# Kernel optimization log

Measured on AMD Instinct MI355X. Metric: run time of the kernel, lower is better.

## Reference

```python
import jax, jax.numpy as jnp
import numpy as np

WIN = 7                      # window_size[0] == window_size[1]
N_TOK = WIN * WIN            # 49 tokens per window
PRETRAIN = 12                # pretrain_window_size
LOG8 = float(np.log(8.0))


def _relative_position_index():
    # tf.meshgrid default 'xy' indexing == np.meshgrid default
    gh, gw = np.meshgrid(np.arange(WIN), np.arange(WIN))
    coords = np.stack([gh, gw], 0).reshape(2, -1)            # [2, N]
    rel = coords[:, :, None] - coords[:, None, :]            # [2, N, N]
    rel = rel.transpose(1, 2, 0)                             # [N, N, 2]
    ry = (rel[..., 0] + WIN - 1) * (2 * WIN - 1)
    rx = rel[..., 1] + WIN - 1
    return jnp.asarray((ry + rx).reshape(-1), dtype=jnp.int32)   # [N*N]


def _relative_coords_table():
    ch = np.arange(-(WIN - 1), WIN, dtype=np.float32)
    gh, gw = np.meshgrid(ch, ch)                             # 'xy' indexing
    t = np.stack([gh, gw], axis=-1)[None]                    # [1, 2W-1, 2W-1, 2]
    t = t / (PRETRAIN - 1)                                   # first divide
    t = t * (8.0 / (PRETRAIN - 1))                           # scale (as in source)
    t = np.sign(t) * np.log1p(np.abs(t)) / LOG8
    return jnp.asarray(t, dtype=jnp.float32)


REL_IDX = _relative_position_index()
COORDS_TABLE = _relative_coords_table()


def _l2_normalize(t, eps=1e-12):
    return t * jax.lax.rsqrt(jnp.maximum(jnp.sum(t * t, axis=-1, keepdims=True), eps))


def setup_inputs() -> dict:
    key = jax.random.key(0)
    ks = jax.random.split(key, 12)
    Bw, N, C, H, RPE_H = 2048, N_TOK, 512, 16, 512
    s = 0.02
    return {
        "x": jax.random.normal(ks[0], (Bw, N, C), jnp.float32),
        "mask": jax.random.normal(ks[1], (64, N, N), jnp.float32),
        "qkv_w": jax.random.normal(ks[2], (C, 3 * C), jnp.float32) * s,
        "q_bias": jnp.zeros((C,), jnp.float32),
        "v_bias": jnp.zeros((C,), jnp.float32),
        "logit_scale": jnp.full((H, 1, 1), np.log(10.0), jnp.float32),
        "rpe_w1": jax.random.normal(ks[3], (2, RPE_H), jnp.float32) * s,
        "rpe_b1": jnp.zeros((RPE_H,), jnp.float32),
        "rpe_w2": jax.random.normal(ks[4], (RPE_H, H), jnp.float32) * s,
        "proj_w": jax.random.normal(ks[5], (C, C), jnp.float32) * s,
        "proj_b": jnp.zeros((C,), jnp.float32),
    }


def reference(x, mask, qkv_w, q_bias, v_bias, logit_scale,
              rpe_w1, rpe_b1, rpe_w2, proj_w, proj_b):
    Bw, N, C = x.shape
    H = logit_scale.shape[0]
    hd = C // H

    qkv_bias = jnp.concatenate([q_bias, jnp.zeros_like(v_bias), v_bias])
    qkv = x @ qkv_w + qkv_bias                          # [Bw, N, 3C]
    qkv = qkv.reshape(Bw, N, 3, H, hd).transpose(2, 0, 3, 1, 4)
    q, k, v = qkv[0], qkv[1], qkv[2]                    # [Bw, H, N, hd]

    scale = jnp.exp(jnp.minimum(logit_scale, jnp.log(1.0 / 0.01)))  # [H,1,1]
    q = _l2_normalize(q)
    k = _l2_normalize(k)
    attn = jnp.einsum('bhnd,bhmd->bhnm', q, k) * scale  # [Bw, H, N, N]

    # RPE MLP on the (2W-1)^2 coords table, then gather per token pair
    h1 = jax.nn.relu(COORDS_TABLE @ rpe_w1 + rpe_b1)
    bias_table = (h1 @ rpe_w2).reshape(-1, H)           # [(2W-1)^2, H]
    pb = bias_table[REL_IDX].reshape(N, N, H).transpose(2, 0, 1)  # [H, N, N]
    attn = attn + 16.0 * jax.nn.sigmoid(pb)[None]

    nW = mask.shape[0]
    attn = attn.reshape(Bw // nW, nW, H, N, N) + mask[None, :, None]
    attn = attn.reshape(Bw, H, N, N)

    attn = jax.nn.softmax(attn, axis=-1)
    out = jnp.einsum('bhnm,bhmd->bnhd', attn, v).reshape(Bw, N, C)
    return out @ proj_w + proj_b
```

## Files before the change

### kernel.cpp

```cpp
#include <hip/hip_runtime.h>
#include <cstdint>

#define NTOK 49
#define CDIM 512
#define BW 2048
#define MROWS (BW * NTOK)
#define QKVN 1536

typedef __attribute__((ext_vector_type(4))) float f32x4;
typedef __attribute__((ext_vector_type(8))) short s16x8;
typedef __attribute__((ext_vector_type(2))) unsigned int u32x2;

__device__ __forceinline__ uint16_t f2b(float f) {
  uint32_t u = __float_as_uint(f);
  u += 0x7fffu + ((u >> 16) & 1u);
  return (uint16_t)(u >> 16);
}
__device__ __forceinline__ float b2f(uint16_t h) {
  return __uint_as_float(((uint32_t)h) << 16);
}

#define GLOAD_LDS16(gp, lp)                                                    \
  __builtin_amdgcn_global_load_lds(                                            \
      (__attribute__((address_space(1))) void*)(gp),                           \
      (__attribute__((address_space(3))) void*)(lp), 16, 0, 0)

__global__ __launch_bounds__(256) void cvt_x_kernel(const float* __restrict__ x,
                                                    uint16_t* __restrict__ xb) {
  long i = ((long)blockIdx.x * 256 + threadIdx.x) * 4;
  f32x4 v = *(const f32x4*)(x + i);
  uint64_t p = (uint64_t)f2b(v[0]) | ((uint64_t)f2b(v[1]) << 16) |
               ((uint64_t)f2b(v[2]) << 32) | ((uint64_t)f2b(v[3]) << 48);
  *(uint64_t*)(xb + i) = p;
}

__global__ __launch_bounds__(256) void prep_weights(
    const float* __restrict__ qkv_w, const float* __restrict__ proj_w,
    const float* __restrict__ q_bias, const float* __restrict__ v_bias,
    uint16_t* __restrict__ qkv_wT, uint16_t* __restrict__ proj_wT,
    float* __restrict__ qkv_bias) {
  int i = blockIdx.x * 256 + threadIdx.x;
  if (i < QKVN * CDIM) {
    int nn = i / CDIM, kk = i % CDIM;
    qkv_wT[i] = f2b(qkv_w[(long)kk * QKVN + nn]);
  }
  if (i < CDIM * CDIM) {
    int nn = i / CDIM, kk = i % CDIM;
    proj_wT[i] = f2b(proj_w[(long)kk * CDIM + nn]);
  }
  if (i < QKVN) {
    float bv = (i < 512) ? q_bias[i] : (i < 1024 ? 0.f : v_bias[i - 1024]);
    qkv_bias[i] = bv;
  }
}

__global__ __launch_bounds__(256) void rpe_table(const float* __restrict__ w1,
                                                 const float* __restrict__ b1,
                                                 const float* __restrict__ w2,
                                                 float* __restrict__ bias16) {
  int i = blockIdx.x * 256 + threadIdx.x;
  if (i >= 169 * 16) return;
  int f = i >> 4, h = i & 15;
  float d0 = (float)((f % 13) - 6);
  float d1 = (float)((f / 13) - 6);
  const float inv_log8 = 0.4808983469629878f;
  float v0 = (d0 / 11.0f) * (8.0f / 11.0f);
  float v1 = (d1 / 11.0f) * (8.0f / 11.0f);
  float f0 = copysignf(log1pf(fabsf(v0)) * inv_log8, v0);
  if (v0 == 0.f) f0 = 0.f;
  float f1 = copysignf(log1pf(fabsf(v1)) * inv_log8, v1);
  if (v1 == 0.f) f1 = 0.f;
  float acc = 0.f;
  for (int k = 0; k < 512; ++k) {
    float h1 = fmaxf(f0 * w1[k] + f1 * w1[512 + k] + b1[k], 0.f);
    acc += h1 * w2[k * 16 + h];
  }
  bias16[i] = 16.f / (1.f + expf(-acc));
}

__global__ __launch_bounds__(256) void build_tiles(
    const float* __restrict__ mask, const float* __restrict__ bias16,
    float* __restrict__ mask_t, float* __restrict__ bias_t) {
  int bid = blockIdx.x;
  int l = threadIdx.x >> 2, j = threadIdx.x & 3;
  int gg = l >> 4, cc = l & 15;
  if (bid < 1024) {
    int w = bid >> 4, tile = bid & 15;
    int mt = tile >> 2, nt = tile & 3;
    int q = nt * 16 + cc, k = mt * 16 + gg * 4 + j;
    float v;
    if (k >= 49) v = -1e30f;
    else if (q >= 49) v = 0.f;
    else v = mask[(long)w * 2401 + q * 49 + k];
    mask_t[(long)bid * 256 + threadIdx.x] = v;
  } else {
    int idx = bid - 1024;
    int h = idx >> 4, tile = idx & 15;
    int mt = tile >> 2, nt = tile & 3;
    int q = nt * 16 + cc, k = mt * 16 + gg * 4 + j;
    float v = 0.f;
    if (q < 49 && k < 49) {
      int ridx = (q % 7 - k % 7 + 6) * 13 + (q / 7 - k / 7 + 6);
      v = bias16[ridx * 16 + h];
    }
    bias_t[(long)idx * 256 + threadIdx.x] = v;
  }
}


#define STAGE_A(tile, half, buf)                                               \
  {                                                                            \
    const uint16_t* s_ = srcA + (half) * (128L * 512) + (long)(tile) * 64;     \
    uint16_t* d_ = &lds[(buf) * 32768 + (half) * 8192 + tid * 8];              \
    GLOAD_LDS16(s_, d_);                                                       \
    GLOAD_LDS16(s_ + 64 * 512, d_ + 4096);                                     \
  }

#define STAGE_B(tile, half, buf)                                               \
  {                                                                            \
    const uint16_t* s_ = srcB + (half) * (128L * 512) + (long)(tile) * 64;     \
    uint16_t* d_ = &lds[(buf) * 32768 + 16384 + (half) * 8192 + tid * 8];      \
    GLOAD_LDS16(s_, d_);                                                       \
    GLOAD_LDS16(s_ + 64 * 512, d_ + 4096);                                     \
  }

#define VM4 asm volatile("s_waitcnt vmcnt(4)" ::: "memory");
#define VM0 asm volatile("s_waitcnt vmcnt(0)" ::: "memory");

#define PHASE(buf, q, STAGES, TAIL)                                            \
  {                                                                            \
    s16x8 a00 = *(const s16x8*)&lds[(buf)*32768 + arow + (2*(q))*1024 + ax0];  \
    s16x8 a01 = *(const s16x8*)&lds[(buf)*32768 + arow + (2*(q))*1024 + ax1];  \
    s16x8 a10 = *(const s16x8*)&lds[(buf)*32768 + arow + (2*(q)+1)*1024 + ax0];\
    s16x8 a11 = *(const s16x8*)&lds[(buf)*32768 + arow + (2*(q)+1)*1024 + ax1];\
    if ((q) == 0) {                                                            \
      _Pragma("unroll")                                                        \
      for (int nf = 0; nf < 4; ++nf) {                                         \
        bfr0[nf] = *(const s16x8*)&lds[(buf)*32768 + brow_ + nf*1024 + ax0];   \
        bfr1[nf] = *(const s16x8*)&lds[(buf)*32768 + brow_ + nf*1024 + ax1];   \
      }                                                                        \
    }                                                                          \
    STAGES                                                                     \
    __builtin_amdgcn_s_barrier();                                              \
    asm volatile("s_waitcnt lgkmcnt(0)" ::: "memory");                         \
    __builtin_amdgcn_sched_barrier(0);                                         \
    __builtin_amdgcn_s_setprio(1);                                             \
    _Pragma("unroll")                                                          \
    for (int nf = 0; nf < 4; ++nf) {                                           \
      acc[2*(q)][nf] = __builtin_amdgcn_mfma_f32_16x16x32_bf16(                \
          a00, bfr0[nf], acc[2*(q)][nf], 0, 0, 0);                             \
      acc[2*(q)][nf] = __builtin_amdgcn_mfma_f32_16x16x32_bf16(                \
          a01, bfr1[nf], acc[2*(q)][nf], 0, 0, 0);                             \
      acc[2*(q)+1][nf] = __builtin_amdgcn_mfma_f32_16x16x32_bf16(              \
          a10, bfr0[nf], acc[2*(q)+1][nf], 0, 0, 0);                           \
      acc[2*(q)+1][nf] = __builtin_amdgcn_mfma_f32_16x16x32_bf16(              \
          a11, bfr1[nf], acc[2*(q)+1][nf], 0, 0, 0);                           \
    }                                                                          \
    __builtin_amdgcn_s_setprio(0);                                             \
    TAIL                                                                       \
    __builtin_amdgcn_s_barrier();                                              \
  }

template <int EPI>
__global__ __launch_bounds__(512, 2) void gemm8p(const uint16_t* __restrict__ A,
                                                 const uint16_t* __restrict__ BT,
                                                 const float* __restrict__ bias,
                                                 void* __restrict__ Cout,
                                                 int N, int ntn) {
  __shared__ uint16_t lds[2 * 32768];
  const int tid = threadIdx.x;
  const int wave = tid >> 6, lane = tid & 63;
  const int wm = wave >> 2, wn = wave & 3;
  const int c = lane & 15, g = lane >> 4;

  const int bid = blockIdx.x;
  const int nwg = gridDim.x;
  const int wg = (bid & 7) * (nwg >> 3) + (bid >> 3);
  const int mt = wg / ntn, nt = wg % ntn;
  const long brow = (long)mt * 256;
  const int bcol = nt * 256;

  const int lr0 = tid >> 3;
  const int chunk = tid & 7;
  const int scol = (chunk ^ (lr0 & 7)) * 8;
  const uint16_t* srcA = A + (brow + lr0) * 512 + scol;
  const uint16_t* srcB = BT + ((long)bcol + lr0) * 512 + scol;

  const int arow = wm * 8192 + c * 64;
  const int brow_ = 16384 + (wn >> 1) * 8192 + ((wn & 1) * 64 + c) * 64;
  const int ax0 = (g * 8) ^ ((c & 7) * 8);
  const int ax1 = (32 + g * 8) ^ ((c & 7) * 8);

  f32x4 acc[8][4];
#pragma unroll
  for (int i = 0; i < 8; ++i)
#pragma unroll
    for (int j = 0; j < 4; ++j) acc[i][j] = f32x4{0.f, 0.f, 0.f, 0.f};
  s16x8 bfr0[4], bfr1[4];

  STAGE_A(0, 0, 0); STAGE_A(0, 1, 0);
  STAGE_B(0, 0, 0); STAGE_B(0, 1, 0);
  STAGE_B(1, 0, 1); STAGE_B(1, 1, 1);
  asm volatile("s_waitcnt vmcnt(4)" ::: "memory");
  __builtin_amdgcn_s_barrier();

  for (int i = 0; i < 3; ++i) {
    const int t0 = 2 * i;
    PHASE(0, 0, STAGE_A(t0 + 1, 0, 1), )
    PHASE(0, 1, STAGE_A(t0 + 1, 1, 1), )
    PHASE(0, 2, STAGE_B(t0 + 2, 0, 0), )
    PHASE(0, 3, STAGE_B(t0 + 2, 1, 0), VM4)
    PHASE(1, 0, STAGE_A(t0 + 2, 0, 0), )
    PHASE(1, 1, STAGE_A(t0 + 2, 1, 0), )
    PHASE(1, 2, STAGE_B(t0 + 3, 0, 1), )
    PHASE(1, 3, STAGE_B(t0 + 3, 1, 1), VM4)
  }
  PHASE(0, 0, STAGE_A(7, 0, 1), )
  PHASE(0, 1, STAGE_A(7, 1, 1), )
  PHASE(0, 2, , )
  PHASE(0, 3, , VM0)
  PHASE(1, 0, , )
  PHASE(1, 1, , )
  PHASE(1, 2, , )
  PHASE(1, 3, , )

#pragma unroll
  for (int mf = 0; mf < 8; ++mf) {
#pragma unroll
    for (int nf = 0; nf < 4; ++nf) {
      const int col = bcol + wn * 64 + nf * 16 + c;
      const float bv = bias[col];
#pragma unroll
      for (int r = 0; r < 4; ++r) {
        const long grow = brow + wm * 128 + mf * 16 + g * 4 + r;
        const float v = acc[mf][nf][r] + bv;
        if (EPI == 0)
          ((uint16_t*)Cout)[grow * N + col] = f2b(v);
        else
          ((float*)Cout)[grow * N + col] = v;
      }
    }
  }
}

__global__ __launch_bounds__(256) void attn_mfma(
    const uint16_t* __restrict__ qkv,
    const float* __restrict__ logit_scale,
    const float* __restrict__ bias_t,
    const float* __restrict__ mask_t,
    uint16_t* __restrict__ outb) {
  __shared__ uint16_t Vs[4][2048];
  __shared__ uint16_t P[4][64 * 72];
  const int tid = threadIdx.x;
  const int wave = tid >> 6, lane = tid & 63;
  const int g = lane >> 4, c = lane & 15;
  const int b = blockIdx.x >> 2;
  const int h = ((blockIdx.x & 3) << 2) | wave;
  const long rbase = (long)b * 49;

  uint16_t* vdst = Vs[wave];
#pragma unroll
  for (int i = 0; i < 4; ++i) {
    int chunk = i * 64 + lane;
    int row = chunk >> 2, part = chunk & 3;
    if (row > 48) { row = 0; part = 0; }
    GLOAD_LDS16(qkv + (rbase + row) * QKVN + 1024 + h * 32 + part * 8,
                vdst + i * 512 + lane * 8);
  }

  const long qoff = rbase * QKVN + h * 32;
  s16x8 kf[4], qf[4];
#pragma unroll
  for (int t = 0; t < 4; ++t) {
    int row = t * 16 + c;
    s16x8 kv = {}, qv = {};
    if (row < 49) {
      qv = *(const s16x8*)(qkv + qoff + (long)row * QKVN + g * 8);
      kv = *(const s16x8*)(qkv + qoff + (long)row * QKVN + 512 + g * 8);
    }
    float kfv[8], qfv[8];
    float kss = 0.f, qss = 0.f;
#pragma unroll
    for (int m = 0; m < 8; ++m) {
      kfv[m] = b2f((uint16_t)kv[m]); kss += kfv[m] * kfv[m];
      qfv[m] = b2f((uint16_t)qv[m]); qss += qfv[m] * qfv[m];
    }
    kss += __shfl_xor(kss, 16); kss += __shfl_xor(kss, 32);
    qss += __shfl_xor(qss, 16); qss += __shfl_xor(qss, 32);
    float kr = rsqrtf(fmaxf(kss, 1e-12f));
    float qr = rsqrtf(fmaxf(qss, 1e-12f));
#pragma unroll
    for (int m = 0; m < 8; ++m) {
      kv[m] = (short)f2b(kfv[m] * kr);
      qv[m] = (short)f2b(qfv[m] * qr);
    }
    kf[t] = kv; qf[t] = qv;
  }

  f32x4 s[4][4];
#pragma unroll
  for (int mt = 0; mt < 4; ++mt)
#pragma unroll
    for (int nt = 0; nt < 4; ++nt)
      s[mt][nt] = __builtin_amdgcn_mfma_f32_16x16x32_bf16(
          kf[mt], qf[nt], f32x4{0.f, 0.f, 0.f, 0.f}, 0, 0, 0);

  const float scale = __expf(fminf(logit_scale[h], 4.6051702f));
  const float* bt = bias_t + (long)h * 4096;
  const float* mk = mask_t + (long)(b & 63) * 4096;
#pragma unroll
  for (int mt = 0; mt < 4; ++mt)
#pragma unroll
    for (int nt = 0; nt < 4; ++nt) {
      int tile = mt * 4 + nt;
      f32x4 eb = *(const f32x4*)(bt + tile * 256 + lane * 4);
      f32x4 em = *(const f32x4*)(mk + tile * 256 + lane * 4);
#pragma unroll
      for (int j = 0; j < 4; ++j)
        s[mt][nt][j] = s[mt][nt][j] * scale + eb[j] + em[j];
    }

#pragma unroll
  for (int nt = 0; nt < 4; ++nt) {
    float mx = -3.0e38f;
#pragma unroll
    for (int mt = 0; mt < 4; ++mt)
#pragma unroll
      for (int j = 0; j < 4; ++j) mx = fmaxf(mx, s[mt][nt][j]);
    mx = fmaxf(mx, __shfl_xor(mx, 16));
    mx = fmaxf(mx, __shfl_xor(mx, 32));
    float sum = 0.f;
#pragma unroll
    for (int mt = 0; mt < 4; ++mt)
#pragma unroll
      for (int j = 0; j < 4; ++j) {
        float e = __expf(s[mt][nt][j] - mx);
        s[mt][nt][j] = e; sum += e;
      }
    sum += __shfl_xor(sum, 16);
    sum += __shfl_xor(sum, 32);
    float inv = 1.0f / sum;
#pragma unroll
    for (int mt = 0; mt < 4; ++mt)
#pragma unroll
      for (int j = 0; j < 4; ++j) s[mt][nt][j] *= inv;
  }

  uint16_t* pw = P[wave];
#pragma unroll
  for (int mt = 0; mt < 4; ++mt)
#pragma unroll
    for (int nt = 0; nt < 4; ++nt) {
      unsigned lo = (unsigned)f2b(s[mt][nt][0]) | ((unsigned)f2b(s[mt][nt][1]) << 16);
      unsigned hi = (unsigned)f2b(s[mt][nt][2]) | ((unsigned)f2b(s[mt][nt][3]) << 16);
      int q = nt * 16 + c;
      int kb = (mt * 16 + g * 4) * 2;
      int addr = q * 144 + (kb ^ ((q & 7) << 4));
      *(u32x2*)((char*)pw + addr) = u32x2{lo, hi};
    }
  __syncthreads();

  f32x4 o[4][2];
#pragma unroll
  for (int qt = 0; qt < 4; ++qt)
#pragma unroll
    for (int dt = 0; dt < 2; ++dt) o[qt][dt] = f32x4{0.f, 0.f, 0.f, 0.f};

#pragma unroll
  for (int ks = 0; ks < 2; ++ks) {
    s16x8 vf[2];
#pragma unroll
    for (int dt = 0; dt < 2; ++dt) {
      int d = dt * 16 + c;
      s16x8 vv;
#pragma unroll
      for (int jj = 0; jj < 8; ++jj) {
        int k = ks * 32 + g * 8 + jj;
        vv[jj] = (short)vdst[k * 32 + d];
      }
      vf[dt] = vv;
    }
#pragma unroll
    for (int qt = 0; qt < 4; ++qt) {
      int q = qt * 16 + c;
      int kbyte = (ks * 64 + g * 16) ^ ((q & 7) << 4);
      s16x8 pf = *(const s16x8*)((const char*)pw + q * 144 + kbyte);
#pragma unroll
      for (int dt = 0; dt < 2; ++dt)
        o[qt][dt] = __builtin_amdgcn_mfma_f32_16x16x32_bf16(pf, vf[dt],
                                                            o[qt][dt], 0, 0, 0);
    }
  }

#pragma unroll
  for (int qt = 0; qt < 4; ++qt) {
    int q0 = qt * 16 + g * 4;
#pragma unroll
    for (int dt = 0; dt < 2; ++dt) {
      int d = dt * 16 + c;
#pragma unroll
      for (int j = 0; j < 4; ++j) {
        int q = q0 + j;
        if (q < 49)
          outb[(rbase + q) * 512 + h * 32 + d] = f2b(o[qt][dt][j]);
      }
    }
  }
}

extern "C" void kernel_launch(void* const* d_in, const int* in_sizes, int n_in,
                              void* d_out, int out_size, void* d_ws,
                              size_t ws_size, hipStream_t stream) {
  const float* x = (const float*)d_in[0];
  const float* mask = (const float*)d_in[1];
  const float* qkv_w = (const float*)d_in[2];
  const float* q_bias = (const float*)d_in[3];
  const float* v_bias = (const float*)d_in[4];
  const float* logit_scale = (const float*)d_in[5];
  const float* rpe_w1 = (const float*)d_in[6];
  const float* rpe_b1 = (const float*)d_in[7];
  const float* rpe_w2 = (const float*)d_in[8];
  const float* proj_w = (const float*)d_in[9];
  const float* proj_b = (const float*)d_in[10];

  char* ws = (char*)d_ws;
  uint16_t* xb       = (uint16_t*)ws;
  uint16_t* qkvbuf   = (uint16_t*)(ws + 102760448L);
  uint16_t* qkv_wT   = (uint16_t*)(ws + 411041792L);
  uint16_t* proj_wT  = (uint16_t*)(ws + 412614656L);
  float*    qkv_bias = (float*)(ws + 413138944L);
  float*    bias16   = (float*)(ws + 413145088L);
  float*    bias_t   = (float*)(ws + 413155904L);
  float*    mask_t   = (float*)(ws + 413418048L);

  cvt_x_kernel<<<50176, 256, 0, stream>>>(x, xb);
  prep_weights<<<3072, 256, 0, stream>>>(qkv_w, proj_w, q_bias, v_bias, qkv_wT,
                                         proj_wT, qkv_bias);
  rpe_table<<<11, 256, 0, stream>>>(rpe_w1, rpe_b1, rpe_w2, bias16);
  build_tiles<<<1280, 256, 0, stream>>>(mask, bias16, mask_t, bias_t);

  gemm8p<0><<<2352, 512, 0, stream>>>(xb, qkv_wT, qkv_bias, qkvbuf, QKVN, 6);
  attn_mfma<<<8192, 256, 0, stream>>>(qkvbuf, logit_scale, bias_t, mask_t, xb);
  gemm8p<1><<<784, 512, 0, stream>>>(xb, proj_wT, proj_b, d_out, CDIM, 2);
}
```

Baseline: 547.2 us.

## Transpose softmax probabilities in registers via ds_permute instead of LDS staging

The attention kernel no longer writes the bf16 probability matrix to a per-wave LDS buffer and reads it back as the A operand. Instead it reshuffles the packed values across lanes with ds_permute, computing S one column tile at a time and fusing the bias, mask and softmax into that loop. The per-wave P buffer and the __syncthreads are removed, replaced by an explicit vmcnt wait for the async V load. It also sets launch_bounds to 4 blocks and raises s_setprio around the MFMA groups. This lowers LDS use and LDS traffic, but the lane-permutation logic is intricate, and the register budget is tighter under the new occupancy hint.

```diff
diff --git a/kernel.cpp b/kernel.cpp
--- a/kernel.cpp
+++ b/kernel.cpp
@@ -9,6 +9,7 @@
 
 typedef __attribute__((ext_vector_type(4))) float f32x4;
 typedef __attribute__((ext_vector_type(8))) short s16x8;
+typedef __attribute__((ext_vector_type(4))) unsigned int u32x4;
 typedef __attribute__((ext_vector_type(2))) unsigned int u32x2;
 
 __device__ __forceinline__ uint16_t f2b(float f) {
@@ -243,14 +244,13 @@
   }
 }
 
-__global__ __launch_bounds__(256) void attn_mfma(
+__global__ __launch_bounds__(256, 4) void attn_mfma(
     const uint16_t* __restrict__ qkv,
     const float* __restrict__ logit_scale,
     const float* __restrict__ bias_t,
     const float* __restrict__ mask_t,
     uint16_t* __restrict__ outb) {
   __shared__ uint16_t Vs[4][2048];
-  __shared__ uint16_t P[4][64 * 72];
   const int tid = threadIdx.x;
   const int wave = tid >> 6, lane = tid & 63;
   const int g = lane >> 4, c = lane & 15;
@@ -297,36 +297,43 @@
     kf[t] = kv; qf[t] = qv;
   }
 
-  f32x4 s[4][4];
-#pragma unroll
-  for (int mt = 0; mt < 4; ++mt)
-#pragma unroll
-    for (int nt = 0; nt < 4; ++nt)
-      s[mt][nt] = __builtin_amdgcn_mfma_f32_16x16x32_bf16(
-          kf[mt], qf[nt], f32x4{0.f, 0.f, 0.f, 0.f}, 0, 0, 0);
-
   const float scale = __expf(fminf(logit_scale[h], 4.6051702f));
   const float* bt = bias_t + (long)h * 4096;
   const float* mk = mask_t + (long)(b & 63) * 4096;
-#pragma unroll
-  for (int mt = 0; mt < 4; ++mt)
-#pragma unroll
-    for (int nt = 0; nt < 4; ++nt) {
+
+  u32x4 aT[4][2];
+  const int dstlo = (c + 16 * (g >> 1)) * 4;
+  const int dsthi = (c + 16 * (2 + (g >> 1))) * 4;
+  const bool godd = (g & 1) != 0;
+  const bool low = (lane < 32);
+
+#pragma unroll
+  for (int nt = 0; nt < 4; ++nt) {
+    f32x4 eb[4], em[4];
+#pragma unroll
+    for (int mt = 0; mt < 4; ++mt) {
       int tile = mt * 4 + nt;
-      f32x4 eb = *(const f32x4*)(bt + tile * 256 + lane * 4);
-      f32x4 em = *(const f32x4*)(mk + tile * 256 + lane * 4);
+      eb[mt] = *(const f32x4*)(bt + tile * 256 + lane * 4);
+      em[mt] = *(const f32x4*)(mk + tile * 256 + lane * 4);
+    }
+    f32x4 sv[4];
+    __builtin_amdgcn_s_setprio(1);
+#pragma unroll
+    for (int mt = 0; mt < 4; ++mt)
+      sv[mt] = __builtin_amdgcn_mfma_f32_16x16x32_bf16(
+          kf[mt], qf[nt], f32x4{0.f, 0.f, 0.f, 0.f}, 0, 0, 0);
+    __builtin_amdgcn_s_setprio(0);
+#pragma unroll
+    for (int mt = 0; mt < 4; ++mt)
 #pragma unroll
       for (int j = 0; j < 4; ++j)
-        s[mt][nt][j] = s[mt][nt][j] * scale + eb[j] + em[j];
-    }
-
-#pragma unroll
-  for (int nt = 0; nt < 4; ++nt) {
+        sv[mt][j] = sv[mt][j] * scale + eb[mt][j] + em[mt][j];
+
     float mx = -3.0e38f;
 #pragma unroll
     for (int mt = 0; mt < 4; ++mt)
 #pragma unroll
-      for (int j = 0; j < 4; ++j) mx = fmaxf(mx, s[mt][nt][j]);
+      for (int j = 0; j < 4; ++j) mx = fmaxf(mx, sv[mt][j]);
     mx = fmaxf(mx, __shfl_xor(mx, 16));
     mx = fmaxf(mx, __shfl_xor(mx, 32));
     float sum = 0.f;
@@ -334,8 +341,8 @@
     for (int mt = 0; mt < 4; ++mt)
 #pragma unroll
       for (int j = 0; j < 4; ++j) {
-        float e = __expf(s[mt][nt][j] - mx);
-        s[mt][nt][j] = e; sum += e;
+        float e = __expf(sv[mt][j] - mx);
+        sv[mt][j] = e; sum += e;
       }
     sum += __shfl_xor(sum, 16);
     sum += __shfl_xor(sum, 32);
@@ -343,22 +350,30 @@
 #pragma unroll
     for (int mt = 0; mt < 4; ++mt)
 #pragma unroll
-      for (int j = 0; j < 4; ++j) s[mt][nt][j] *= inv;
-  }
-
-  uint16_t* pw = P[wave];
-#pragma unroll
-  for (int mt = 0; mt < 4; ++mt)
-#pragma unroll
-    for (int nt = 0; nt < 4; ++nt) {
-      unsigned lo = (unsigned)f2b(s[mt][nt][0]) | ((unsigned)f2b(s[mt][nt][1]) << 16);
-      unsigned hi = (unsigned)f2b(s[mt][nt][2]) | ((unsigned)f2b(s[mt][nt][3]) << 16);
-      int q = nt * 16 + c;
-      int kb = (mt * 16 + g * 4) * 2;
-      int addr = q * 144 + (kb ^ ((q & 7) << 4));
-      *(u32x2*)((char*)pw + addr) = u32x2{lo, hi};
-    }
-  __syncthreads();
+      for (int j = 0; j < 4; ++j) sv[mt][j] *= inv;
+
+    unsigned pk[4][2];
+#pragma unroll
+    for (int mt = 0; mt < 4; ++mt) {
+      pk[mt][0] = (unsigned)f2b(sv[mt][0]) | ((unsigned)f2b(sv[mt][1]) << 16);
+      pk[mt][1] = (unsigned)f2b(sv[mt][2]) | ((unsigned)f2b(sv[mt][3]) << 16);
+    }
+#pragma unroll
+    for (int x = 0; x < 2; ++x)
+#pragma unroll
+      for (int K = 0; K < 2; ++K) {
+        int vA = godd ? (int)pk[2 * K + 1][x] : (int)pk[2 * K][x];
+        int dA = godd ? dsthi : dstlo;
+        int rA = __builtin_amdgcn_ds_permute(dA, vA);
+        int vB = godd ? (int)pk[2 * K][x] : (int)pk[2 * K + 1][x];
+        int dB = godd ? dstlo : dsthi;
+        int rB = __builtin_amdgcn_ds_permute(dB, vB);
+        aT[nt][K][x]     = (unsigned)(low ? rA : rB);
+        aT[nt][K][2 + x] = (unsigned)(low ? rB : rA);
+      }
+  }
+
+  asm volatile("s_waitcnt vmcnt(0)" ::: "memory");
 
   f32x4 o[4][2];
 #pragma unroll
@@ -380,16 +395,16 @@
       }
       vf[dt] = vv;
     }
+    __builtin_amdgcn_s_setprio(1);
 #pragma unroll
     for (int qt = 0; qt < 4; ++qt) {
-      int q = qt * 16 + c;
-      int kbyte = (ks * 64 + g * 16) ^ ((q & 7) << 4);
-      s16x8 pf = *(const s16x8*)((const char*)pw + q * 144 + kbyte);
+      s16x8 pf = __builtin_bit_cast(s16x8, aT[qt][ks]);
 #pragma unroll
       for (int dt = 0; dt < 2; ++dt)
         o[qt][dt] = __builtin_amdgcn_mfma_f32_16x16x32_bf16(pf, vf[dt],
                                                             o[qt][dt], 0, 0, 0);
     }
+    __builtin_amdgcn_s_setprio(0);
   }
 
 #pragma unroll
```

Measured after the change: 562.0 us. +2.7%, slower.
